# Kernel optimization log

Measured on AMD Instinct MI355X. Metric: run time of the kernel, lower is better.

The kernel has to match this reference:

```python
import jax, jax.numpy as jnp
import numpy as np

DIM = 512
H = 8
HD = DIM // H
B = 1
S = 4096
SCALE = HD ** -0.5


def setup_inputs() -> dict:
    key = jax.random.key(0)
    k1, k2, k3, k4, k5 = jax.random.split(key, 5)
    bound = DIM ** -0.5
    x = jax.random.normal(k1, (B, S, DIM), dtype=jnp.float32)
    q_param = jax.random.uniform(k2, (DIM, H, HD), dtype=jnp.float32, minval=-bound, maxval=bound)
    k_param = jax.random.uniform(k3, (DIM, H, HD), dtype=jnp.float32, minval=-bound, maxval=bound)
    v_param = jax.random.uniform(k4, (DIM, H, HD), dtype=jnp.float32, minval=-bound, maxval=bound)
    p_param = jax.random.uniform(k5, (H, HD, DIM), dtype=jnp.float32, minval=-bound, maxval=bound)
    return {"x": x, "q_param": q_param, "k_param": k_param, "v_param": v_param, "p_param": p_param}


def reference(x, q_param, k_param, v_param, p_param):
    q = jnp.einsum('bsc,chd->bshd', x, q_param) * SCALE
    k = jnp.einsum('btc,chd->bthd', x, k_param)
    v = jnp.einsum('btc,chd->bthd', x, v_param)
    attn = jax.nn.softmax(jnp.einsum('bshd,bthd->bhst', q, k), axis=-1)  # [B,H,S,S]
    o = jnp.einsum('bhst,bthd->bshd', attn, v)
    return jnp.einsum('bshd,hdc->bsc', o, p_param)
```

## Files before the change

kernel.cpp:

```cpp
#include <hip/hip_runtime.h>
#include <hip/hip_bf16.h>
#include <stdint.h>

#define S_LEN 4096
#define DIM   512
#define NH    8
#define HD    64
#define NZ    4
#define ZROWS 1024
#define QSCALE 0.18033688011112042f

typedef __attribute__((ext_vector_type(8))) short short8;
typedef __attribute__((ext_vector_type(4))) float f32x4;
typedef __attribute__((ext_vector_type(16))) float f32x16;
typedef __attribute__((ext_vector_type(2))) unsigned uint2v;

__device__ __forceinline__ uint32_t pk2(float lo, float hi) {
  union { __hip_bfloat162 h; uint32_t u; } cv;
  cv.h = __float22bfloat162_rn(float2{lo, hi});
  return cv.u;
}
__device__ __forceinline__ ushort bf1(float x) {
  union { __hip_bfloat16 b; ushort u; } cv;
  cv.b = __float2bfloat16(x);
  return cv.u;
}
__device__ __forceinline__ float bf2f(ushort u) {
  union { uint32_t u; float f; } cv;
  cv.u = (uint32_t)u << 16;
  return cv.f;
}
__device__ __forceinline__ float fexp2(float x) {
  float r;
  asm("v_exp_f32 %0, %1" : "=v"(r) : "v"(x));
  return r;
}

__global__ __launch_bounds__(256)
void cast_x(const float* __restrict__ src, ushort* __restrict__ dst) {
  const int i = (blockIdx.x * 256 + threadIdx.x) * 8;
  const float4 a = *reinterpret_cast<const float4*>(src + i);
  const float4 b = *reinterpret_cast<const float4*>(src + i + 4);
  uint4 o;
  o.x = pk2(a.x, a.y); o.y = pk2(a.z, a.w);
  o.z = pk2(b.x, b.y); o.w = pk2(b.z, b.w);
  *reinterpret_cast<uint4*>(dst + i) = o;
}

__global__ __launch_bounds__(256)
void transpose_w(const float* __restrict__ qp, const float* __restrict__ kp,
                 const float* __restrict__ vp, const float* __restrict__ pp,
                 ushort* __restrict__ wbT, ushort* __restrict__ ppT) {
  __shared__ float L[64][65];
  const int z = blockIdx.z;
  const float* src = (z == 0) ? qp : (z == 1) ? kp : (z == 2) ? vp : pp;
  ushort* dst = (z < 3) ? (wbT + (size_t)z * 512 * 512) : ppT;
  const float scale = (z == 0) ? QSCALE : 1.0f;
  const int k0 = blockIdx.x * 64, n0 = blockIdx.y * 64;
  const int r = threadIdx.x >> 2, c0 = (threadIdx.x & 3) * 16;

#pragma unroll
  for (int j = 0; j < 4; ++j) {
    const float4 v =
        *reinterpret_cast<const float4*>(&src[(k0 + r) * 512 + n0 + c0 + 4 * j]);
    L[r][c0 + 4 * j + 0] = v.x * scale;
    L[r][c0 + 4 * j + 1] = v.y * scale;
    L[r][c0 + 4 * j + 2] = v.z * scale;
    L[r][c0 + 4 * j + 3] = v.w * scale;
  }
  __syncthreads();

  uint4 u0, u1;
  u0.x = pk2(L[c0 + 0][r], L[c0 + 1][r]);
  u0.y = pk2(L[c0 + 2][r], L[c0 + 3][r]);
  u0.z = pk2(L[c0 + 4][r], L[c0 + 5][r]);
  u0.w = pk2(L[c0 + 6][r], L[c0 + 7][r]);
  u1.x = pk2(L[c0 + 8][r], L[c0 + 9][r]);
  u1.y = pk2(L[c0 + 10][r], L[c0 + 11][r]);
  u1.z = pk2(L[c0 + 12][r], L[c0 + 13][r]);
  u1.w = pk2(L[c0 + 14][r], L[c0 + 15][r]);
  ushort* d = dst + (size_t)(n0 + r) * 512 + k0 + c0;
  *reinterpret_cast<uint4*>(d) = u0;
  *reinterpret_cast<uint4*>(d + 8) = u1;
}

template <int MODE>
__global__ __launch_bounds__(256)
void gemm_bf16(const ushort* __restrict__ A, const ushort* __restrict__ Bt,
               void* __restrict__ Cout) {
  __shared__ __align__(16) unsigned char lds[24576];
  const int tid = threadIdx.x;
  const int m0 = blockIdx.x * 128, n0 = blockIdx.y * 64;
  const int lane = tid & 63, w = tid >> 6;
  const int wm = w >> 1, wn = w & 1;
  const int q = lane & 15, g = lane >> 4;
  f32x4 acc[4][2] = {};

  const int ar = tid >> 1, ah = tid & 1;
  const int br = tid >> 2, bq = tid & 3;

  for (int k0 = 0; k0 < 512; k0 += 64) {
    const ushort* ag = A + (size_t)(m0 + ar) * 512 + k0 + ah * 32;
    const uint4 a0 = *reinterpret_cast<const uint4*>(ag);
    const uint4 a1 = *reinterpret_cast<const uint4*>(ag + 8);
    const uint4 a2 = *reinterpret_cast<const uint4*>(ag + 16);
    const uint4 a3 = *reinterpret_cast<const uint4*>(ag + 24);
    const ushort* bg = Bt + (size_t)(n0 + br) * 512 + k0 + bq * 16;
    const uint4 b0 = *reinterpret_cast<const uint4*>(bg);
    const uint4 b1 = *reinterpret_cast<const uint4*>(bg + 8);
    __syncthreads();
    {
      unsigned char* ab = lds + ar * 128;
      const int asw = (ar & 7) << 4;
      *reinterpret_cast<uint4*>(ab + ((ah * 64 + 0) ^ asw)) = a0;
      *reinterpret_cast<uint4*>(ab + ((ah * 64 + 16) ^ asw)) = a1;
      *reinterpret_cast<uint4*>(ab + ((ah * 64 + 32) ^ asw)) = a2;
      *reinterpret_cast<uint4*>(ab + ((ah * 64 + 48) ^ asw)) = a3;
      unsigned char* bb = lds + 16384 + br * 128;
      const int bsw = (br & 7) << 4;
      *reinterpret_cast<uint4*>(bb + ((bq * 32 + 0) ^ bsw)) = b0;
      *reinterpret_cast<uint4*>(bb + ((bq * 32 + 16) ^ bsw)) = b1;
    }
    __syncthreads();

#pragma unroll
    for (int ks = 0; ks < 2; ++ks) {
      short8 bf[2];
#pragma unroll
      for (int ni = 0; ni < 2; ++ni) {
        const int rn = wn * 32 + ni * 16 + q;
        bf[ni] = *reinterpret_cast<const short8*>(
            lds + 16384 + rn * 128 + ((64 * ks + 16 * g) ^ ((rn & 7) << 4)));
      }
#pragma unroll
      for (int mi = 0; mi < 4; ++mi) {
        const int rm = wm * 64 + mi * 16 + q;
        const short8 af = *reinterpret_cast<const short8*>(
            lds + rm * 128 + ((64 * ks + 16 * g) ^ ((rm & 7) << 4)));
#pragma unroll
        for (int ni = 0; ni < 2; ++ni)
          acc[mi][ni] = __builtin_amdgcn_mfma_f32_16x16x32_bf16(
              af, bf[ni], acc[mi][ni], 0, 0, 0);
      }
    }
  }

  if (MODE == 0) {
    ushort* C = (ushort*)Cout;
    const int which = n0 >> 9;
#pragma unroll
    for (int ni = 0; ni < 2; ++ni) {
      const int n = n0 + wn * 32 + ni * 16 + q;
      const int rem = n & 511, hh = rem >> 6, d = rem & 63;
      if (which == 2) {
        ushort* base = C + (size_t)(2 * NH + hh) * (size_t)(S_LEN * HD) +
                       (size_t)d * S_LEN;
#pragma unroll
        for (int mi = 0; mi < 4; ++mi) {
          const int s = m0 + wm * 64 + mi * 16 + 4 * g;
          uint2 pw;
          pw.x = pk2(acc[mi][ni][0], acc[mi][ni][1]);
          pw.y = pk2(acc[mi][ni][2], acc[mi][ni][3]);
          *reinterpret_cast<uint2*>(base + s) = pw;
        }
      } else {
        ushort* base =
            C + ((size_t)which * NH + hh) * (size_t)(S_LEN * HD) + d;
#pragma unroll
        for (int mi = 0; mi < 4; ++mi) {
          const int s = m0 + wm * 64 + mi * 16 + 4 * g;
#pragma unroll
          for (int r = 0; r < 4; ++r)
            base[(size_t)(s + r) * HD] = bf1(acc[mi][ni][r]);
        }
      }
    }
  } else {
    float* C = (float*)Cout;
#pragma unroll
    for (int ni = 0; ni < 2; ++ni) {
      const int n = n0 + wn * 32 + ni * 16 + q;
#pragma unroll
      for (int mi = 0; mi < 4; ++mi) {
        const int s = m0 + wm * 64 + mi * 16 + 4 * g;
#pragma unroll
        for (int r = 0; r < 4; ++r)
          C[(size_t)(s + r) * 512 + n] = acc[mi][ni][r];
      }
    }
  }
}

__global__ __launch_bounds__(256, 2)
void attn_mfma32(const ushort* __restrict__ QKV, ushort* __restrict__ Opart,
                 float2* __restrict__ ML) {
  __shared__ __align__(16) unsigned char lds[32768];
  const int tid = threadIdx.x;
  const int combo = blockIdx.x;
  const int h = combo & 7, z = combo >> 3;
  const int qb = blockIdx.y;
  const int lane = tid & 63, w = tid >> 6;
  const int r31 = lane & 31, hh = lane >> 5;

  const size_t plane = (size_t)S_LEN * HD;
  const ushort* Qp = QKV + (size_t)h * plane;
  const ushort* Kp = QKV + (size_t)(NH + h) * plane;
  const ushort* Vp = QKV + (size_t)(2 * NH + h) * plane;

  const int qbase = qb * 256 + w * 64;
  const int qrowA = qbase + r31, qrowB = qbase + 32 + r31;

  short8 qfA[4], qfB[4];
  {
    const ushort* qa = Qp + (size_t)qrowA * HD + 8 * hh;
    const ushort* qbp = Qp + (size_t)qrowB * HD + 8 * hh;
#pragma unroll
    for (int ks = 0; ks < 4; ++ks) {
      qfA[ks] = *reinterpret_cast<const short8*>(qa + 16 * ks);
      qfB[ks] = *reinterpret_cast<const short8*>(qbp + 16 * ks);
    }
  }

  int roff[4];
#pragma unroll
  for (int ks = 0; ks < 4; ++ks)
    roff[ks] = (((2 * ks + hh) << 4) ^ ((r31 & 7) << 4));
  const int rbase = r31 * 128;

  const int trow = tid >> 2, seg = tid & 3;
  const int tsw = (trow & 7) << 4;
  const int wk0 = trow * 128 + ((seg * 32) ^ tsw);
  const int wk1 = trow * 128 + ((seg * 32 + 16) ^ tsw);
  const ushort* kgbase = Kp + (size_t)(z * ZROWS + trow) * HD + seg * 16;
  const ushort* vgbase = Vp + (size_t)trow * S_LEN + z * ZROWS + seg * 16;

  f32x16 oA[2] = {}, oB[2] = {};
  float mA = -1e30f, lA = 0.f, mB = -1e30f, lB = 0.f;

  uint4 kst0 = *reinterpret_cast<const uint4*>(kgbase);
  uint4 kst1 = *reinterpret_cast<const uint4*>(kgbase + 8);
  uint4 vst0 = *reinterpret_cast<const uint4*>(vgbase);
  uint4 vst1 = *reinterpret_cast<const uint4*>(vgbase + 8);

  for (int t = 0; t < 16; ++t) {
    const int po = (t & 1) << 14;
    *reinterpret_cast<uint4*>(lds + (wk0 | po)) = kst0;
    *reinterpret_cast<uint4*>(lds + (wk1 | po)) = kst1;
    *reinterpret_cast<uint4*>(lds + ((8192 + wk0) | po)) = vst0;
    *reinterpret_cast<uint4*>(lds + ((8192 + wk1) | po)) = vst1;
    __syncthreads();

    const int tn = (t + 1) & 15;
    kst0 = *reinterpret_cast<const uint4*>(kgbase + tn * 4096);
    kst1 = *reinterpret_cast<const uint4*>(kgbase + tn * 4096 + 8);
    vst0 = *reinterpret_cast<const uint4*>(vgbase + tn * 64);
    vst1 = *reinterpret_cast<const uint4*>(vgbase + tn * 64 + 8);

    f32x16 sA0 = {}, sA1 = {}, sB0 = {}, sB1 = {};
    __builtin_amdgcn_s_setprio(1);
#pragma unroll
    for (int ks = 0; ks < 4; ++ks) {
      const short8 af0 = *reinterpret_cast<const short8*>(
          lds + ((rbase + roff[ks]) | po));
      const short8 af1 = *reinterpret_cast<const short8*>(
          lds + ((4096 + rbase + roff[ks]) | po));
      sA0 = __builtin_amdgcn_mfma_f32_32x32x16_bf16(af0, qfA[ks], sA0, 0, 0, 0);
      sB0 = __builtin_amdgcn_mfma_f32_32x32x16_bf16(af0, qfB[ks], sB0, 0, 0, 0);
      sA1 = __builtin_amdgcn_mfma_f32_32x32x16_bf16(af1, qfA[ks], sA1, 0, 0, 0);
      sB1 = __builtin_amdgcn_mfma_f32_32x32x16_bf16(af1, qfB[ks], sB1, 0, 0, 0);
    }
    __builtin_amdgcn_s_setprio(0);

    {
      float mv[8];
#pragma unroll
      for (int i = 0; i < 8; ++i)
        mv[i] = fmaxf(fmaxf(sA0[i], sA0[i + 8]), fmaxf(sA1[i], sA1[i + 8]));
#pragma unroll
      for (int i = 0; i < 4; ++i) mv[i] = fmaxf(mv[i], mv[i + 4]);
      float mx = fmaxf(fmaxf(mv[0], mv[1]), fmaxf(mv[2], mv[3]));
      mx = fmaxf(mx, __shfl_xor(mx, 32));
      const bool grow = mx > mA + 8.0f;
      if (__any(grow)) {
        const float mn = grow ? mx : mA;
        const float alpha = grow ? fexp2(mA - mn) : 1.0f;
        lA *= alpha;
#pragma unroll
        for (int i = 0; i < 16; ++i) { oA[0][i] *= alpha; oA[1][i] *= alpha; }
        mA = mn;
      }
      float r0 = 0.f, r1 = 0.f, r2 = 0.f, r3 = 0.f;
#pragma unroll
      for (int i = 0; i < 16; i += 4) {
        sA0[i + 0] = fexp2(sA0[i + 0] - mA); r0 += sA0[i + 0];
        sA0[i + 1] = fexp2(sA0[i + 1] - mA); r1 += sA0[i + 1];
        sA0[i + 2] = fexp2(sA0[i + 2] - mA); r2 += sA0[i + 2];
        sA0[i + 3] = fexp2(sA0[i + 3] - mA); r3 += sA0[i + 3];
        sA1[i + 0] = fexp2(sA1[i + 0] - mA); r0 += sA1[i + 0];
        sA1[i + 1] = fexp2(sA1[i + 1] - mA); r1 += sA1[i + 1];
        sA1[i + 2] = fexp2(sA1[i + 2] - mA); r2 += sA1[i + 2];
        sA1[i + 3] = fexp2(sA1[i + 3] - mA); r3 += sA1[i + 3];
      }
      lA += (r0 + r1) + (r2 + r3);
    }
    {
      float mv[8];
#pragma unroll
      for (int i = 0; i < 8; ++i)
        mv[i] = fmaxf(fmaxf(sB0[i], sB0[i + 8]), fmaxf(sB1[i], sB1[i + 8]));
#pragma unroll
      for (int i = 0; i < 4; ++i) mv[i] = fmaxf(mv[i], mv[i + 4]);
      float mx = fmaxf(fmaxf(mv[0], mv[1]), fmaxf(mv[2], mv[3]));
      mx = fmaxf(mx, __shfl_xor(mx, 32));
      const bool grow = mx > mB + 8.0f;
      if (__any(grow)) {
        const float mn = grow ? mx : mB;
        const float alpha = grow ? fexp2(mB - mn) : 1.0f;
        lB *= alpha;
#pragma unroll
        for (int i = 0; i < 16; ++i) { oB[0][i] *= alpha; oB[1][i] *= alpha; }
        mB = mn;
      }
      float r0 = 0.f, r1 = 0.f, r2 = 0.f, r3 = 0.f;
#pragma unroll
      for (int i = 0; i < 16; i += 4) {
        sB0[i + 0] = fexp2(sB0[i + 0] - mB); r0 += sB0[i + 0];
        sB0[i + 1] = fexp2(sB0[i + 1] - mB); r1 += sB0[i + 1];
        sB0[i + 2] = fexp2(sB0[i + 2] - mB); r2 += sB0[i + 2];
        sB0[i + 3] = fexp2(sB0[i + 3] - mB); r3 += sB0[i + 3];
        sB1[i + 0] = fexp2(sB1[i + 0] - mB); r0 += sB1[i + 0];
        sB1[i + 1] = fexp2(sB1[i + 1] - mB); r1 += sB1[i + 1];
        sB1[i + 2] = fexp2(sB1[i + 2] - mB); r2 += sB1[i + 2];
        sB1[i + 3] = fexp2(sB1[i + 3] - mB); r3 += sB1[i + 3];
      }
      lB += (r0 + r1) + (r2 + r3);
    }

    short8 pfA[4], pfB[4];
#pragma unroll
    for (int e = 0; e < 2; ++e) {
      const int bb = 2 * e;
      {
        const uint32_t u00 = pk2(sA0[4 * bb + 0], sA0[4 * bb + 1]);
        const uint32_t u01 = pk2(sA0[4 * bb + 2], sA0[4 * bb + 3]);
        const uint32_t u10 = pk2(sA0[4 * bb + 4], sA0[4 * bb + 5]);
        const uint32_t u11 = pk2(sA0[4 * bb + 6], sA0[4 * bb + 7]);
        const uint2v se0 =
            __builtin_amdgcn_permlane32_swap(u00, u10, false, false);
        const uint2v se1 =
            __builtin_amdgcn_permlane32_swap(u01, u11, false, false);
        uint32_t fr[4] = {se0.x, se1.x, se0.y, se1.y};
        pfA[e] = *reinterpret_cast<short8*>(fr);
      }
      {
        const uint32_t u00 = pk2(sA1[4 * bb + 0], sA1[4 * bb + 1]);
        const uint32_t u01 = pk2(sA1[4 * bb + 2], sA1[4 * bb + 3]);
        const uint32_t u10 = pk2(sA1[4 * bb + 4], sA1[4 * bb + 5]);
        const uint32_t u11 = pk2(sA1[4 * bb + 6], sA1[4 * bb + 7]);
        const uint2v se0 =
            __builtin_amdgcn_permlane32_swap(u00, u10, false, false);
        const uint2v se1 =
            __builtin_amdgcn_permlane32_swap(u01, u11, false, false);
        uint32_t fr[4] = {se0.x, se1.x, se0.y, se1.y};
        pfA[2 + e] = *reinterpret_cast<short8*>(fr);
      }
      {
        const uint32_t u00 = pk2(sB0[4 * bb + 0], sB0[4 * bb + 1]);
        const uint32_t u01 = pk2(sB0[4 * bb + 2], sB0[4 * bb + 3]);
        const uint32_t u10 = pk2(sB0[4 * bb + 4], sB0[4 * bb + 5]);
        const uint32_t u11 = pk2(sB0[4 * bb + 6], sB0[4 * bb + 7]);
        const uint2v se0 =
            __builtin_amdgcn_permlane32_swap(u00, u10, false, false);
        const uint2v se1 =
            __builtin_amdgcn_permlane32_swap(u01, u11, false, false);
        uint32_t fr[4] = {se0.x, se1.x, se0.y, se1.y};
        pfB[e] = *reinterpret_cast<short8*>(fr);
      }
      {
        const uint32_t u00 = pk2(sB1[4 * bb + 0], sB1[4 * bb + 1]);
        const uint32_t u01 = pk2(sB1[4 * bb + 2], sB1[4 * bb + 3]);
        const uint32_t u10 = pk2(sB1[4 * bb + 4], sB1[4 * bb + 5]);
        const uint32_t u11 = pk2(sB1[4 * bb + 6], sB1[4 * bb + 7]);
        const uint2v se0 =
            __builtin_amdgcn_permlane32_swap(u00, u10, false, false);
        const uint2v se1 =
            __builtin_amdgcn_permlane32_swap(u01, u11, false, false);
        uint32_t fr[4] = {se0.x, se1.x, se0.y, se1.y};
        pfB[2 + e] = *reinterpret_cast<short8*>(fr);
      }
    }

    __builtin_amdgcn_s_setprio(1);
#pragma unroll
    for (int dt = 0; dt < 2; ++dt)
#pragma unroll
      for (int kg = 0; kg < 4; ++kg) {
        const short8 vf = *reinterpret_cast<const short8*>(
            lds + ((8192 + (32 * dt + r31) * 128 +
                    (((32 * kg + 16 * hh)) ^ ((r31 & 7) << 4))) |
                   po));
        oA[dt] = __builtin_amdgcn_mfma_f32_32x32x16_bf16(vf, pfA[kg], oA[dt],
                                                         0, 0, 0);
        oB[dt] = __builtin_amdgcn_mfma_f32_32x32x16_bf16(vf, pfB[kg], oB[dt],
                                                         0, 0, 0);
      }
    __builtin_amdgcn_s_setprio(0);
  }

  lA += __shfl_xor(lA, 32);
  lB += __shfl_xor(lB, 32);

  if (lane < 32) {
    ML[(size_t)combo * S_LEN + qrowA] = float2{mA, lA};
    ML[(size_t)combo * S_LEN + qrowB] = float2{mB, lB};
  }
  ushort* obA = Opart + ((size_t)combo * S_LEN + qrowA) * HD;
  ushort* obB = Opart + ((size_t)combo * S_LEN + qrowB) * HD;
#pragma unroll
  for (int dt = 0; dt < 2; ++dt)
#pragma unroll
    for (int rq = 0; rq < 4; ++rq) {
      const int d = 32 * dt + 8 * rq + 4 * hh;
      uint2 pwA, pwB;
      pwA.x = pk2(oA[dt][4 * rq + 0], oA[dt][4 * rq + 1]);
      pwA.y = pk2(oA[dt][4 * rq + 2], oA[dt][4 * rq + 3]);
      pwB.x = pk2(oB[dt][4 * rq + 0], oB[dt][4 * rq + 1]);
      pwB.y = pk2(oB[dt][4 * rq + 2], oB[dt][4 * rq + 3]);
      *reinterpret_cast<uint2*>(obA + d) = pwA;
      *reinterpret_cast<uint2*>(obB + d) = pwB;
    }
}

__global__ __launch_bounds__(256)
void combine(const ushort* __restrict__ Opart, const float2* __restrict__ ML,
             ushort* __restrict__ ob) {
  const int t = threadIdx.x;
  const int qq = t & 63, ds = t >> 6;
  const int q = blockIdx.x * 64 + qq;
  const int h = blockIdx.y;

  float m = -1e30f, mz[NZ], lz[NZ];
#pragma unroll
  for (int z = 0; z < NZ; ++z) {
    const float2 v = ML[(size_t)(z * 8 + h) * S_LEN + q];
    mz[z] = v.x; lz[z] = v.y;
    m = fmaxf(m, v.x);
  }
  float wz[NZ], l = 0.f;
#pragma unroll
  for (int z = 0; z < NZ; ++z) {
    wz[z] = fexp2(mz[z] - m);
    l += wz[z] * lz[z];
  }
  const float inv = 1.0f / l;
#pragma unroll
  for (int z = 0; z < NZ; ++z) wz[z] *= inv;

  float acc[16];
#pragma unroll
  for (int i = 0; i < 16; ++i) acc[i] = 0.f;
#pragma unroll
  for (int z = 0; z < NZ; ++z) {
    const ushort* src =
        Opart + (((size_t)(z * 8 + h) * S_LEN) + q) * HD + ds * 16;
    const uint4 u0 = *reinterpret_cast<const uint4*>(src);
    const uint4 u1 = *reinterpret_cast<const uint4*>(src + 8);
    const ushort* e0 = reinterpret_cast<const ushort*>(&u0);
    const ushort* e1 = reinterpret_cast<const ushort*>(&u1);
#pragma unroll
    for (int i = 0; i < 8; ++i) {
      acc[i] = fmaf(wz[z], bf2f(e0[i]), acc[i]);
      acc[i + 8] = fmaf(wz[z], bf2f(e1[i]), acc[i + 8]);
    }
  }
  uint32_t pk[8];
#pragma unroll
  for (int i = 0; i < 8; ++i)
    pk[i] = pk2(acc[2 * i], acc[2 * i + 1]);
  ushort* dst = ob + (size_t)q * DIM + h * 64 + ds * 16;
  *reinterpret_cast<uint4*>(dst) = *reinterpret_cast<uint4*>(pk);
  *reinterpret_cast<uint4*>(dst + 8) = *reinterpret_cast<uint4*>(pk + 4);
}

extern "C" void kernel_launch(void* const* d_in, const int* in_sizes, int n_in,
                              void* d_out, int out_size, void* d_ws, size_t ws_size,
                              hipStream_t stream) {
  const float* x  = (const float*)d_in[0];
  const float* qp = (const float*)d_in[1];
  const float* kp = (const float*)d_in[2];
  const float* vp = (const float*)d_in[3];
  const float* pp = (const float*)d_in[4];
  float* out = (float*)d_out;

  unsigned char* ws = (unsigned char*)d_ws;
  ushort* xb    = (ushort*)(ws);
  ushort* qkvb  = (ushort*)(ws + ((size_t)4 << 20));
  ushort* ob    = (ushort*)(ws + ((size_t)16 << 20));
  ushort* wbT   = (ushort*)(ws + ((size_t)20 << 20));
  ushort* ppT   = (ushort*)(ws + ((size_t)22 << 20));
  ushort* opart = (ushort*)(ws + ((size_t)23 << 20));
  float2* ml    = (float2*)(ws + ((size_t)39 << 20));

  cast_x<<<dim3(1024), dim3(256), 0, stream>>>(x, xb);
  transpose_w<<<dim3(8, 8, 4), dim3(256), 0, stream>>>(qp, kp, vp, pp, wbT, ppT);
  gemm_bf16<0><<<dim3(32, 24), dim3(256), 0, stream>>>(xb, wbT, qkvb);
  attn_mfma32<<<dim3(32, 16), dim3(256), 0, stream>>>(qkvb, opart, ml);
  combine<<<dim3(64, 8), dim3(256), 0, stream>>>(opart, ml, ob);
  gemm_bf16<1><<<dim3(32, 8), dim3(256), 0, stream>>>(ob, ppT, out);
}
```

Before: 94.29 us.

## Fuse split-KV combine into output GEMM and software-pipeline PV with next QK

Removes the separate combine kernel by having the output projection GEMM (new MODE 2) merge the four partial attention outputs with their max/sum weights while loading its A tile. The attention kernel is restructured to issue the QK MFMAs of the current tile before the PV MFMAs of the previous tile, with a triple-buffered V region in a larger LDS allocation. The aim is to cut one launch and an intermediate round trip, and to overlap softmax latency with matrix work. In exchange, each output GEMM block recomputes the combine eight times (once per N tile), and the larger LDS footprint may limit occupancy.

```diff
diff --git a/kernel.cpp b/kernel.cpp
--- a/kernel.cpp
+++ b/kernel.cpp
@@ -87,7 +87,7 @@
 template <int MODE>
 __global__ __launch_bounds__(256)
 void gemm_bf16(const ushort* __restrict__ A, const ushort* __restrict__ Bt,
-               void* __restrict__ Cout) {
+               void* __restrict__ Cout, const float2* __restrict__ ML) {
   __shared__ __align__(16) unsigned char lds[24576];
   const int tid = threadIdx.x;
   const int m0 = blockIdx.x * 128, n0 = blockIdx.y * 64;
@@ -100,11 +100,68 @@
   const int br = tid >> 2, bq = tid & 3;
 
   for (int k0 = 0; k0 < 512; k0 += 64) {
-    const ushort* ag = A + (size_t)(m0 + ar) * 512 + k0 + ah * 32;
-    const uint4 a0 = *reinterpret_cast<const uint4*>(ag);
-    const uint4 a1 = *reinterpret_cast<const uint4*>(ag + 8);
-    const uint4 a2 = *reinterpret_cast<const uint4*>(ag + 16);
-    const uint4 a3 = *reinterpret_cast<const uint4*>(ag + 24);
+    uint4 a0, a1, a2, a3;
+    if constexpr (MODE != 2) {
+      const ushort* ag = A + (size_t)(m0 + ar) * 512 + k0 + ah * 32;
+      a0 = *reinterpret_cast<const uint4*>(ag);
+      a1 = *reinterpret_cast<const uint4*>(ag + 8);
+      a2 = *reinterpret_cast<const uint4*>(ag + 16);
+      a3 = *reinterpret_cast<const uint4*>(ag + 24);
+    } else {
+      const int srow = m0 + ar;
+      const int hd = k0 >> 6;
+      const int d0 = ah * 32;
+      float mz[4], lz[4];
+      float mM = -1e30f;
+#pragma unroll
+      for (int z = 0; z < NZ; ++z) {
+        const float2 v = ML[(size_t)(z * 8 + hd) * S_LEN + srow];
+        mz[z] = v.x; lz[z] = v.y;
+        mM = fmaxf(mM, v.x);
+      }
+      float wz[4], l = 0.f;
+#pragma unroll
+      for (int z = 0; z < NZ; ++z) {
+        wz[z] = fexp2(mz[z] - mM);
+        l += wz[z] * lz[z];
+      }
+      const float inv = 1.0f / l;
+#pragma unroll
+      for (int z = 0; z < NZ; ++z) wz[z] *= inv;
+
+      float a[32];
+#pragma unroll
+      for (int j = 0; j < 32; ++j) a[j] = 0.f;
+#pragma unroll
+      for (int z = 0; z < NZ; ++z) {
+        const ushort* src =
+            A + ((size_t)(z * 8 + hd) * S_LEN + srow) * HD + d0;
+        const uint4 u0 = *reinterpret_cast<const uint4*>(src);
+        const uint4 u1 = *reinterpret_cast<const uint4*>(src + 8);
+        const uint4 u2 = *reinterpret_cast<const uint4*>(src + 16);
+        const uint4 u3 = *reinterpret_cast<const uint4*>(src + 24);
+        const ushort* e0 = reinterpret_cast<const ushort*>(&u0);
+        const ushort* e1 = reinterpret_cast<const ushort*>(&u1);
+        const ushort* e2 = reinterpret_cast<const ushort*>(&u2);
+        const ushort* e3 = reinterpret_cast<const ushort*>(&u3);
+#pragma unroll
+        for (int j = 0; j < 8; ++j) {
+          a[j] = fmaf(wz[z], bf2f(e0[j]), a[j]);
+          a[j + 8] = fmaf(wz[z], bf2f(e1[j]), a[j + 8]);
+          a[j + 16] = fmaf(wz[z], bf2f(e2[j]), a[j + 16]);
+          a[j + 24] = fmaf(wz[z], bf2f(e3[j]), a[j + 24]);
+        }
+      }
+      uint4 pa[4];
+#pragma unroll
+      for (int g4 = 0; g4 < 4; ++g4) {
+        pa[g4].x = pk2(a[8 * g4 + 0], a[8 * g4 + 1]);
+        pa[g4].y = pk2(a[8 * g4 + 2], a[8 * g4 + 3]);
+        pa[g4].z = pk2(a[8 * g4 + 4], a[8 * g4 + 5]);
+        pa[g4].w = pk2(a[8 * g4 + 6], a[8 * g4 + 7]);
+      }
+      a0 = pa[0]; a1 = pa[1]; a2 = pa[2]; a3 = pa[3];
+    }
     const ushort* bg = Bt + (size_t)(n0 + br) * 512 + k0 + bq * 16;
     const uint4 b0 = *reinterpret_cast<const uint4*>(bg);
     const uint4 b1 = *reinterpret_cast<const uint4*>(bg + 8);
@@ -145,7 +202,7 @@
     }
   }
 
-  if (MODE == 0) {
+  if constexpr (MODE == 0) {
     ushort* C = (ushort*)Cout;
     const int which = n0 >> 9;
 #pragma unroll
@@ -194,7 +251,7 @@
 __global__ __launch_bounds__(256, 2)
 void attn_mfma32(const ushort* __restrict__ QKV, ushort* __restrict__ Opart,
                  float2* __restrict__ ML) {
-  __shared__ __align__(16) unsigned char lds[32768];
+  __shared__ __align__(16) unsigned char lds[40960];
   const int tid = threadIdx.x;
   const int combo = blockIdx.x;
   const int h = combo & 7, z = combo >> 3;
@@ -236,41 +293,61 @@
 
   f32x16 oA[2] = {}, oB[2] = {};
   float mA = -1e30f, lA = 0.f, mB = -1e30f, lB = 0.f;
+  short8 pfA[4], pfB[4];
+
+  int vfoff[2][4];
+#pragma unroll
+  for (int dt = 0; dt < 2; ++dt)
+#pragma unroll
+    for (int kg = 0; kg < 4; ++kg)
+      vfoff[dt][kg] = (32 * dt + r31) * 128 +
+                      ((32 * kg + 16 * hh) ^ ((r31 & 7) << 4));
 
   uint4 kst0 = *reinterpret_cast<const uint4*>(kgbase);
   uint4 kst1 = *reinterpret_cast<const uint4*>(kgbase + 8);
   uint4 vst0 = *reinterpret_cast<const uint4*>(vgbase);
   uint4 vst1 = *reinterpret_cast<const uint4*>(vgbase + 8);
 
-  for (int t = 0; t < 16; ++t) {
-    const int po = (t & 1) << 14;
-    *reinterpret_cast<uint4*>(lds + (wk0 | po)) = kst0;
-    *reinterpret_cast<uint4*>(lds + (wk1 | po)) = kst1;
-    *reinterpret_cast<uint4*>(lds + ((8192 + wk0) | po)) = vst0;
-    *reinterpret_cast<uint4*>(lds + ((8192 + wk1) | po)) = vst1;
-    __syncthreads();
-
-    const int tn = (t + 1) & 15;
-    kst0 = *reinterpret_cast<const uint4*>(kgbase + tn * 4096);
-    kst1 = *reinterpret_cast<const uint4*>(kgbase + tn * 4096 + 8);
-    vst0 = *reinterpret_cast<const uint4*>(vgbase + tn * 64);
-    vst1 = *reinterpret_cast<const uint4*>(vgbase + tn * 64 + 8);
-
-    f32x16 sA0 = {}, sA1 = {}, sB0 = {}, sB1 = {};
+  int kpoW = 0;
+  int vW = 16384;
+  int vR = 16384;
+
+  f32x16 sA0, sA1, sB0, sB1;
+
+  auto do_qk = [&](int kpo) {
+    sA0 = f32x16{}; sA1 = f32x16{}; sB0 = f32x16{}; sB1 = f32x16{};
     __builtin_amdgcn_s_setprio(1);
 #pragma unroll
     for (int ks = 0; ks < 4; ++ks) {
-      const short8 af0 = *reinterpret_cast<const short8*>(
-          lds + ((rbase + roff[ks]) | po));
-      const short8 af1 = *reinterpret_cast<const short8*>(
-          lds + ((4096 + rbase + roff[ks]) | po));
+      const short8 af0 =
+          *reinterpret_cast<const short8*>(lds + kpo + rbase + roff[ks]);
+      const short8 af1 =
+          *reinterpret_cast<const short8*>(lds + kpo + 4096 + rbase + roff[ks]);
       sA0 = __builtin_amdgcn_mfma_f32_32x32x16_bf16(af0, qfA[ks], sA0, 0, 0, 0);
       sB0 = __builtin_amdgcn_mfma_f32_32x32x16_bf16(af0, qfB[ks], sB0, 0, 0, 0);
       sA1 = __builtin_amdgcn_mfma_f32_32x32x16_bf16(af1, qfA[ks], sA1, 0, 0, 0);
       sB1 = __builtin_amdgcn_mfma_f32_32x32x16_bf16(af1, qfB[ks], sB1, 0, 0, 0);
     }
     __builtin_amdgcn_s_setprio(0);
-
+  };
+
+  auto do_pv = [&](int vpo) {
+    __builtin_amdgcn_s_setprio(1);
+#pragma unroll
+    for (int dt = 0; dt < 2; ++dt)
+#pragma unroll
+      for (int kg = 0; kg < 4; ++kg) {
+        const short8 vf =
+            *reinterpret_cast<const short8*>(lds + vpo + vfoff[dt][kg]);
+        oA[dt] = __builtin_amdgcn_mfma_f32_32x32x16_bf16(vf, pfA[kg], oA[dt],
+                                                         0, 0, 0);
+        oB[dt] = __builtin_amdgcn_mfma_f32_32x32x16_bf16(vf, pfB[kg], oB[dt],
+                                                         0, 0, 0);
+      }
+    __builtin_amdgcn_s_setprio(0);
+  };
+
+  auto do_sm_pack = [&]() {
     {
       float mv[8];
 #pragma unroll
@@ -335,8 +412,6 @@
       }
       lB += (r0 + r1) + (r2 + r3);
     }
-
-    short8 pfA[4], pfB[4];
 #pragma unroll
     for (int e = 0; e < 2; ++e) {
       const int bb = 2 * e;
@@ -389,23 +464,41 @@
         pfB[2 + e] = *reinterpret_cast<short8*>(fr);
       }
     }
-
-    __builtin_amdgcn_s_setprio(1);
-#pragma unroll
-    for (int dt = 0; dt < 2; ++dt)
-#pragma unroll
-      for (int kg = 0; kg < 4; ++kg) {
-        const short8 vf = *reinterpret_cast<const short8*>(
-            lds + ((8192 + (32 * dt + r31) * 128 +
-                    (((32 * kg + 16 * hh)) ^ ((r31 & 7) << 4))) |
-                   po));
-        oA[dt] = __builtin_amdgcn_mfma_f32_32x32x16_bf16(vf, pfA[kg], oA[dt],
-                                                         0, 0, 0);
-        oB[dt] = __builtin_amdgcn_mfma_f32_32x32x16_bf16(vf, pfB[kg], oB[dt],
-                                                         0, 0, 0);
-      }
-    __builtin_amdgcn_s_setprio(0);
+  };
+
+  *reinterpret_cast<uint4*>(lds + kpoW + wk0) = kst0;
+  *reinterpret_cast<uint4*>(lds + kpoW + wk1) = kst1;
+  *reinterpret_cast<uint4*>(lds + vW + wk0) = vst0;
+  *reinterpret_cast<uint4*>(lds + vW + wk1) = vst1;
+  __syncthreads();
+  kst0 = *reinterpret_cast<const uint4*>(kgbase + 4096);
+  kst1 = *reinterpret_cast<const uint4*>(kgbase + 4096 + 8);
+  vst0 = *reinterpret_cast<const uint4*>(vgbase + 64);
+  vst1 = *reinterpret_cast<const uint4*>(vgbase + 64 + 8);
+  do_qk(kpoW);
+  do_sm_pack();
+
+  for (int t = 1; t < 16; ++t) {
+    kpoW ^= 8192;
+    vW = (vW == 32768) ? 16384 : vW + 8192;
+    *reinterpret_cast<uint4*>(lds + kpoW + wk0) = kst0;
+    *reinterpret_cast<uint4*>(lds + kpoW + wk1) = kst1;
+    *reinterpret_cast<uint4*>(lds + vW + wk0) = vst0;
+    *reinterpret_cast<uint4*>(lds + vW + wk1) = vst1;
+    __syncthreads();
+
+    const int tn = (t + 1) & 15;
+    kst0 = *reinterpret_cast<const uint4*>(kgbase + tn * 4096);
+    kst1 = *reinterpret_cast<const uint4*>(kgbase + tn * 4096 + 8);
+    vst0 = *reinterpret_cast<const uint4*>(vgbase + tn * 64);
+    vst1 = *reinterpret_cast<const uint4*>(vgbase + tn * 64 + 8);
+
+    do_qk(kpoW);
+    do_pv(vR);
+    vR = vW;
+    do_sm_pack();
   }
+  do_pv(vR);
 
   lA += __shfl_xor(lA, 32);
   lB += __shfl_xor(lB, 32);
@@ -431,57 +524,6 @@
     }
 }
 
-__global__ __launch_bounds__(256)
-void combine(const ushort* __restrict__ Opart, const float2* __restrict__ ML,
-             ushort* __restrict__ ob) {
-  const int t = threadIdx.x;
-  const int qq = t & 63, ds = t >> 6;
-  const int q = blockIdx.x * 64 + qq;
-  const int h = blockIdx.y;
-
-  float m = -1e30f, mz[NZ], lz[NZ];
-#pragma unroll
-  for (int z = 0; z < NZ; ++z) {
-    const float2 v = ML[(size_t)(z * 8 + h) * S_LEN + q];
-    mz[z] = v.x; lz[z] = v.y;
-    m = fmaxf(m, v.x);
-  }
-  float wz[NZ], l = 0.f;
-#pragma unroll
-  for (int z = 0; z < NZ; ++z) {
-    wz[z] = fexp2(mz[z] - m);
-    l += wz[z] * lz[z];
-  }
-  const float inv = 1.0f / l;
-#pragma unroll
-  for (int z = 0; z < NZ; ++z) wz[z] *= inv;
-
-  float acc[16];
-#pragma unroll
-  for (int i = 0; i < 16; ++i) acc[i] = 0.f;
-#pragma unroll
-  for (int z = 0; z < NZ; ++z) {
-    const ushort* src =
-        Opart + (((size_t)(z * 8 + h) * S_LEN) + q) * HD + ds * 16;
-    const uint4 u0 = *reinterpret_cast<const uint4*>(src);
-    const uint4 u1 = *reinterpret_cast<const uint4*>(src + 8);
-    const ushort* e0 = reinterpret_cast<const ushort*>(&u0);
-    const ushort* e1 = reinterpret_cast<const ushort*>(&u1);
-#pragma unroll
-    for (int i = 0; i < 8; ++i) {
-      acc[i] = fmaf(wz[z], bf2f(e0[i]), acc[i]);
-      acc[i + 8] = fmaf(wz[z], bf2f(e1[i]), acc[i + 8]);
-    }
-  }
-  uint32_t pk[8];
-#pragma unroll
-  for (int i = 0; i < 8; ++i)
-    pk[i] = pk2(acc[2 * i], acc[2 * i + 1]);
-  ushort* dst = ob + (size_t)q * DIM + h * 64 + ds * 16;
-  *reinterpret_cast<uint4*>(dst) = *reinterpret_cast<uint4*>(pk);
-  *reinterpret_cast<uint4*>(dst + 8) = *reinterpret_cast<uint4*>(pk + 4);
-}
-
 extern "C" void kernel_launch(void* const* d_in, const int* in_sizes, int n_in,
                               void* d_out, int out_size, void* d_ws, size_t ws_size,
                               hipStream_t stream) {
@@ -495,7 +537,6 @@
   unsigned char* ws = (unsigned char*)d_ws;
   ushort* xb    = (ushort*)(ws);
   ushort* qkvb  = (ushort*)(ws + ((size_t)4 << 20));
-  ushort* ob    = (ushort*)(ws + ((size_t)16 << 20));
   ushort* wbT   = (ushort*)(ws + ((size_t)20 << 20));
   ushort* ppT   = (ushort*)(ws + ((size_t)22 << 20));
   ushort* opart = (ushort*)(ws + ((size_t)23 << 20));
@@ -503,8 +544,7 @@
 
   cast_x<<<dim3(1024), dim3(256), 0, stream>>>(x, xb);
   transpose_w<<<dim3(8, 8, 4), dim3(256), 0, stream>>>(qp, kp, vp, pp, wbT, ppT);
-  gemm_bf16<0><<<dim3(32, 24), dim3(256), 0, stream>>>(xb, wbT, qkvb);
+  gemm_bf16<0><<<dim3(32, 24), dim3(256), 0, stream>>>(xb, wbT, qkvb, nullptr);
   attn_mfma32<<<dim3(32, 16), dim3(256), 0, stream>>>(qkvb, opart, ml);
-  combine<<<dim3(64, 8), dim3(256), 0, stream>>>(opart, ml, ob);
-  gemm_bf16<1><<<dim3(32, 8), dim3(256), 0, stream>>>(ob, ppT, out);
-}
+  gemm_bf16<2><<<dim3(32, 8), dim3(256), 0, stream>>>(opart, ppT, out, ml);
+}
```

Result: slower. 111.6 us (+18.3%).
